# Optimization experiments

Hardware: AMD Instinct MI355X
Metric: run time of the kernel (lower is better)

Reference implementation:

```python
import jax, jax.numpy as jnp
import numpy as np

NEG_PENALTY = 0.03
B, C_TOTAL, C_LOADED = 2048, 1000, 256


def setup_inputs() -> dict:
    key = jax.random.key(0)
    k1, k2, k3 = jax.random.split(key, 3)
    ranks = jax.random.normal(k1, (B, C_TOTAL), dtype=jnp.float32)
    labels = jax.random.randint(k2, (B, C_TOTAL), 0, 2, dtype=jnp.int32)
    class_ids_loaded = jnp.sort(jax.random.randint(k3, (C_LOADED,), 0, C_TOTAL, dtype=jnp.int64))
    return {"ranks": ranks, "labels": labels, "class_ids_loaded": class_ids_loaded}


def reference(ranks, labels, class_ids_loaded):
    # Select loaded classes: [B, C]
    lab = labels[:, class_ids_loaded].astype(ranks.dtype)
    r = ranks[:, class_ids_loaded]
    pos = lab            # 1 where label == 1 (correct)
    neg = 1.0 - lab      # 1 where label == 0 (wrong)
    # Pairwise hinge: relu(penalty + wrong_rank - correct_rank) over all (correct p, wrong n) pairs.
    # pen[b, p, n] = relu(NEG_PENALTY + r[b, n] - r[b, p]); mask after relu == computing only valid pairs.
    pen = jax.nn.relu(NEG_PENALTY + r[:, None, :] - r[:, :, None])  # [B, C, C]
    total = jnp.einsum('bpn,bp,bn->', pen, pos, neg)
    # Denominator: number of rows with at least one positive label.
    n_valid = jnp.sum(jnp.any(lab == 1.0, axis=1)).astype(ranks.dtype)
    return (total / n_valid).reshape((1,))
```

## Files before the change

### kernel.cpp

```cpp
#include <hip/hip_runtime.h>

#define B_ROWS 2048
#define C_TOTAL 1000
#define C_LOADED 256
#define NEG_PEN 0.03f


__global__ void __launch_bounds__(C_LOADED)
rank_loss_kernel(const float* __restrict__ ranks,
                 const int* __restrict__ labels,
                 const int* __restrict__ ids,
                 float2* __restrict__ pv) {
    __shared__ __align__(16) float negl[264];
    __shared__ float wave_sums[4];
    __shared__ int wave_base[4];
    __shared__ int ncnt;

    const int b = blockIdx.x;
    const int t = threadIdx.x;
    const int lane = t & 63;
    const int wave = t >> 6;

    if (t == 0) ncnt = 0;

    const int c = ids[t];
    const float r = ranks[b * C_TOTAL + c];
    const int lab = labels[b * C_TOTAL + c];
    const bool isneg = (lab == 0);

    const unsigned long long m = __ballot(isneg);
    const int cnt_wave = __popcll(m);
    const int my_pos = __popcll(m & ((1ULL << lane) - 1ULL));

    __syncthreads();
    if (lane == 0) wave_base[wave] = atomicAdd(&ncnt, cnt_wave);
    __syncthreads();

    const int N = ncnt;
    const int Npad = (N + 7) & ~7;
    if (isneg) negl[wave_base[wave] + my_pos] = r + NEG_PEN;
    if (t >= N && t < Npad) negl[t] = -1e30f;
    __syncthreads();

    const float rp = (lab == 1) ? r : 3e30f;

    float a0 = 0.f, a1 = 0.f, a2 = 0.f, a3 = 0.f;
    float a4 = 0.f, a5 = 0.f, a6 = 0.f, a7 = 0.f;
    const float4* n4 = (const float4*)negl;
    const int G = Npad >> 2;
    for (int g = 0; g < G; g += 2) {
        float4 x = n4[g];
        float4 y = n4[g + 1];
        a0 += fmaxf(x.x - rp, 0.0f);
        a1 += fmaxf(x.y - rp, 0.0f);
        a2 += fmaxf(x.z - rp, 0.0f);
        a3 += fmaxf(x.w - rp, 0.0f);
        a4 += fmaxf(y.x - rp, 0.0f);
        a5 += fmaxf(y.y - rp, 0.0f);
        a6 += fmaxf(y.z - rp, 0.0f);
        a7 += fmaxf(y.w - rp, 0.0f);
    }
    float acc = ((a0 + a1) + (a2 + a3)) + ((a4 + a5) + (a6 + a7));

#pragma unroll
    for (int off = 32; off > 0; off >>= 1) {
        acc += __shfl_down(acc, off, 64);
    }
    if (lane == 0) wave_sums[wave] = acc;
    __syncthreads();

    if (t == 0) {
        float s = (wave_sums[0] + wave_sums[1]) + (wave_sums[2] + wave_sums[3]);
        pv[b] = make_float2(s, (N < C_LOADED) ? 1.0f : 0.0f);
    }
}

__global__ void __launch_bounds__(1024)
finalize_kernel(const float4* __restrict__ pv4, float* __restrict__ out) {
    __shared__ float ws_s[16], ws_v[16];
    const int t = threadIdx.x;
    const int lane = t & 63;
    const int wave = t >> 6;

    const float4 v = pv4[t];
    float s = v.x + v.z;
    float nv = v.y + v.w;

#pragma unroll
    for (int off = 32; off > 0; off >>= 1) {
        s  += __shfl_down(s, off, 64);
        nv += __shfl_down(nv, off, 64);
    }
    if (lane == 0) { ws_s[wave] = s; ws_v[wave] = nv; }
    __syncthreads();

    if (t == 0) {
        float ts = 0.f, tv = 0.f;
#pragma unroll
        for (int w = 0; w < 16; ++w) { ts += ws_s[w]; tv += ws_v[w]; }
        out[0] = ts / tv;
    }
}

extern "C" void kernel_launch(void* const* d_in, const int* in_sizes, int n_in,
                              void* d_out, int out_size, void* d_ws, size_t ws_size,
                              hipStream_t stream) {
    const float* ranks  = (const float*)d_in[0];
    const int*   labels = (const int*)d_in[1];
    const int*   ids    = (const int*)d_in[2];
    float* out = (float*)d_out;

    float2* pv = (float2*)d_ws;

    rank_loss_kernel<<<B_ROWS, C_LOADED, 0, stream>>>(ranks, labels, ids, pv);
    finalize_kernel<<<1, 1024, 0, stream>>>((const float4*)pv, out);
}
```

Baseline: 13.65 us.

## Compact positives to skip idle waves and process two rows per block

Each block now handles two rows, loading both rows' ranks and labels up front. Positive ranks are compacted into shared memory alongside negatives, so only the first P threads run the pairwise loop and whole waves can skip it. This targets wasted ALU work from threads holding negatives and per-block launch overhead. The cost is extra syncthreads per row and halved grid parallelism.

```diff
diff --git a/kernel.cpp b/kernel.cpp
--- a/kernel.cpp
+++ b/kernel.cpp
@@ -4,6 +4,8 @@
 #define C_TOTAL 1000
 #define C_LOADED 256
 #define NEG_PEN 0.03f
+#define ROWS 2
+#define GRID (B_ROWS / ROWS)
 
 
 __global__ void __launch_bounds__(C_LOADED)
@@ -12,66 +14,92 @@
                  const int* __restrict__ ids,
                  float2* __restrict__ pv) {
     __shared__ __align__(16) float negl[264];
-    __shared__ float wave_sums[4];
-    __shared__ int wave_base[4];
-    __shared__ int ncnt;
+    __shared__ float posl[256];
+    __shared__ float wave_sums[ROWS][4];
+    __shared__ int wb_n[4], wb_p[4];
+    __shared__ int ncnt[ROWS], pcnt[ROWS];
 
-    const int b = blockIdx.x;
     const int t = threadIdx.x;
     const int lane = t & 63;
     const int wave = t >> 6;
+    const int r0 = blockIdx.x * ROWS;
 
-    if (t == 0) ncnt = 0;
+    if (t == 0) {
+#pragma unroll
+        for (int i = 0; i < ROWS; ++i) { ncnt[i] = 0; pcnt[i] = 0; }
+    }
 
     const int c = ids[t];
-    const float r = ranks[b * C_TOTAL + c];
-    const int lab = labels[b * C_TOTAL + c];
-    const bool isneg = (lab == 0);
-
-    const unsigned long long m = __ballot(isneg);
-    const int cnt_wave = __popcll(m);
-    const int my_pos = __popcll(m & ((1ULL << lane) - 1ULL));
+    const float rv0 = ranks[(size_t)r0 * C_TOTAL + c];
+    const int   lb0 = labels[(size_t)r0 * C_TOTAL + c];
+    const float rv1 = ranks[(size_t)(r0 + 1) * C_TOTAL + c];
+    const int   lb1 = labels[(size_t)(r0 + 1) * C_TOTAL + c];
 
     __syncthreads();
-    if (lane == 0) wave_base[wave] = atomicAdd(&ncnt, cnt_wave);
-    __syncthreads();
 
-    const int N = ncnt;
-    const int Npad = (N + 7) & ~7;
-    if (isneg) negl[wave_base[wave] + my_pos] = r + NEG_PEN;
-    if (t >= N && t < Npad) negl[t] = -1e30f;
-    __syncthreads();
-
-    const float rp = (lab == 1) ? r : 3e30f;
-
-    float a0 = 0.f, a1 = 0.f, a2 = 0.f, a3 = 0.f;
-    float a4 = 0.f, a5 = 0.f, a6 = 0.f, a7 = 0.f;
-    const float4* n4 = (const float4*)negl;
-    const int G = Npad >> 2;
-    for (int g = 0; g < G; g += 2) {
-        float4 x = n4[g];
-        float4 y = n4[g + 1];
-        a0 += fmaxf(x.x - rp, 0.0f);
-        a1 += fmaxf(x.y - rp, 0.0f);
-        a2 += fmaxf(x.z - rp, 0.0f);
-        a3 += fmaxf(x.w - rp, 0.0f);
-        a4 += fmaxf(y.x - rp, 0.0f);
-        a5 += fmaxf(y.y - rp, 0.0f);
-        a6 += fmaxf(y.z - rp, 0.0f);
-        a7 += fmaxf(y.w - rp, 0.0f);
-    }
-    float acc = ((a0 + a1) + (a2 + a3)) + ((a4 + a5) + (a6 + a7));
+    float rv = rv0;
+    int lab = lb0;
 
 #pragma unroll
-    for (int off = 32; off > 0; off >>= 1) {
-        acc += __shfl_down(acc, off, 64);
-    }
-    if (lane == 0) wave_sums[wave] = acc;
-    __syncthreads();
+    for (int i = 0; i < ROWS; ++i) {
+        const bool isneg = (lab == 0);
+        const unsigned long long m = __ballot(isneg);
+        const unsigned long long lm = (1ULL << lane) - 1ULL;
+        const int nneg_w = __popcll(m);
+        const int my_n = __popcll(m & lm);
+        const int my_p = __popcll(~m & lm);
 
-    if (t == 0) {
-        float s = (wave_sums[0] + wave_sums[1]) + (wave_sums[2] + wave_sums[3]);
-        pv[b] = make_float2(s, (N < C_LOADED) ? 1.0f : 0.0f);
+        if (lane == 0) {
+            wb_n[wave] = atomicAdd(&ncnt[i], nneg_w);
+            wb_p[wave] = atomicAdd(&pcnt[i], 64 - nneg_w);
+        }
+        __syncthreads();
+
+        const int N = ncnt[i];
+        const int P = C_LOADED - N;
+        const int Npad = (N + 7) & ~7;
+        if (isneg) negl[wb_n[wave] + my_n] = rv + NEG_PEN;
+        else       posl[wb_p[wave] + my_p] = rv;
+        if (t >= N && t < Npad) negl[t] = -1e30f;
+        __syncthreads();
+
+        float acc = 0.f;
+        if (t < P) {
+            const float rp = posl[t];
+            float a0 = 0.f, a1 = 0.f, a2 = 0.f, a3 = 0.f;
+            float a4 = 0.f, a5 = 0.f, a6 = 0.f, a7 = 0.f;
+            const float4* n4 = (const float4*)negl;
+            const int G = Npad >> 2;
+            for (int g = 0; g < G; g += 2) {
+                float4 x = n4[g];
+                float4 y = n4[g + 1];
+                a0 += fmaxf(x.x - rp, 0.0f);
+                a1 += fmaxf(x.y - rp, 0.0f);
+                a2 += fmaxf(x.z - rp, 0.0f);
+                a3 += fmaxf(x.w - rp, 0.0f);
+                a4 += fmaxf(y.x - rp, 0.0f);
+                a5 += fmaxf(y.y - rp, 0.0f);
+                a6 += fmaxf(y.z - rp, 0.0f);
+                a7 += fmaxf(y.w - rp, 0.0f);
+            }
+            acc = ((a0 + a1) + (a2 + a3)) + ((a4 + a5) + (a6 + a7));
+        }
+
+#pragma unroll
+        for (int off = 32; off > 0; off >>= 1) {
+            acc += __shfl_down(acc, off, 64);
+        }
+        if (lane == 0) wave_sums[i][wave] = acc;
+        __syncthreads();
+
+        if (t == 0) {
+            float s = (wave_sums[i][0] + wave_sums[i][1]) +
+                      (wave_sums[i][2] + wave_sums[i][3]);
+            pv[r0 + i] = make_float2(s, (P > 0) ? 1.0f : 0.0f);
+        }
+
+        rv = rv1;
+        lab = lb1;
     }
 }
 
@@ -112,6 +140,6 @@
 
     float2* pv = (float2*)d_ws;
 
-    rank_loss_kernel<<<B_ROWS, C_LOADED, 0, stream>>>(ranks, labels, ids, pv);
+    rank_loss_kernel<<<GRID, C_LOADED, 0, stream>>>(ranks, labels, ids, pv);
     finalize_kernel<<<1, 1024, 0, stream>>>((const float4*)pv, out);
 }
```

Result: slower. 14.50 us (+6.2%).
